# Performance work log

Measured on AMD Instinct MI355X. Metric: run time of the kernel, lower is better.

Reference implementation:

```python
import jax, jax.numpy as jnp
import numpy as np

B, N, M, C, T, HF, WF = 4, 512, 32, 512, 8, 14, 14
K = 80          # num_classes
P = 7           # ROI pool output size
HID = 1024
IMG = 224


def setup_inputs() -> dict:
    key = jax.random.key(0)
    k0, k1, k2, k3, k4, k5 = jax.random.split(key, 6)
    feature = jax.random.normal(k0, (B, C, T, HF, WF), dtype=jnp.float32)
    # GT boxes: realistic xyxy boxes inside a 224x224 image
    ka, kb = jax.random.split(k1)
    cxy = jax.random.uniform(ka, (B, M, 2), minval=40.0, maxval=180.0)
    wh = jax.random.uniform(kb, (B, M, 2), minval=40.0, maxval=100.0)
    gt_bboxes = jnp.concatenate([cxy - wh / 2, cxy + wh / 2], axis=-1).astype(jnp.float32)
    # Proposals: jittered copies of GT boxes so many pass the IoU>=0.85 fg test
    idx = jnp.arange(N) % M
    base = gt_bboxes[:, idx]                                   # [B,N,4]
    noise = jax.random.normal(k2, (B, N, 4), dtype=jnp.float32) * 1.5
    proposal_bboxes = jnp.clip(base + noise, 0.0, float(IMG))
    gt_classes = (jax.random.uniform(k3, (B, M, K)) < 0.1).astype(jnp.float32)
    W1 = jax.random.normal(k4, (C * P * P, HID), dtype=jnp.float32) * 0.01
    b1 = jnp.zeros((HID,), jnp.float32)
    W2 = jax.random.normal(k5, (HID, K), dtype=jnp.float32) * 0.01
    b2 = jnp.zeros((K,), jnp.float32)
    return {"feature": feature, "proposal_bboxes": proposal_bboxes,
            "gt_bboxes": gt_bboxes, "gt_classes": gt_classes,
            "W1": W1, "b1": b1, "W2": W2, "b2": b2,
            "image_h": IMG, "image_w": IMG}


def _iou(a, b):
    # a [B,N,4], b [B,M,4] xyxy -> [B,N,M]
    lt = jnp.maximum(a[:, :, None, :2], b[:, None, :, :2])
    rb = jnp.minimum(a[:, :, None, 2:], b[:, None, :, 2:])
    wh = jnp.clip(rb - lt, 0.0)
    inter = wh[..., 0] * wh[..., 1]
    area_a = (a[..., 2] - a[..., 0]) * (a[..., 3] - a[..., 1])
    area_b = (b[..., 2] - b[..., 0]) * (b[..., 3] - b[..., 1])
    return inter / (area_a[:, :, None] + area_b[:, None, :] - inter + 1e-8)


def _roi_pool(feat_bhwc, boxes, bidx, sy, sx):
    # feat_bhwc [B,H,W,C]; boxes [R,4] image coords; bilinear 7x7 ROI pooling
    H, W = feat_bhwc.shape[1], feat_bhwc.shape[2]
    x1, y1, x2, y2 = boxes[:, 0] * sx, boxes[:, 1] * sy, boxes[:, 2] * sx, boxes[:, 3] * sy
    g = (jnp.arange(P, dtype=jnp.float32) + 0.5) / P
    ys = y1[:, None] + g[None, :] * (y2 - y1)[:, None]        # [R,P]
    xs = x1[:, None] + g[None, :] * (x2 - x1)[:, None]        # [R,P]
    y = jnp.broadcast_to(ys[:, :, None], (boxes.shape[0], P, P)) - 0.5
    x = jnp.broadcast_to(xs[:, None, :], (boxes.shape[0], P, P)) - 0.5
    y0f = jnp.floor(y); x0f = jnp.floor(x)
    wy = jnp.clip(y - y0f, 0.0, 1.0)[..., None]
    wx = jnp.clip(x - x0f, 0.0, 1.0)[..., None]
    y0 = jnp.clip(y0f, 0, H - 1).astype(jnp.int32)
    y1i = jnp.clip(y0f + 1, 0, H - 1).astype(jnp.int32)
    x0 = jnp.clip(x0f, 0, W - 1).astype(jnp.int32)
    x1i = jnp.clip(x0f + 1, 0, W - 1).astype(jnp.int32)
    bi = bidx[:, None, None]
    gather = lambda yy, xx: feat_bhwc[bi, yy, xx]             # [R,P,P,C]
    out = (gather(y0, x0) * (1 - wy) * (1 - wx) + gather(y0, x1i) * (1 - wy) * wx +
           gather(y1i, x0) * wy * (1 - wx) + gather(y1i, x1i) * wy * wx)
    return out


def reference(feature, proposal_bboxes, gt_bboxes, gt_classes, W1, b1, W2, b2, image_h, image_w):
    # temporal average pool (AvgPool3d over T) -> [B,C,HF,WF]
    feat = feature.mean(axis=2)
    feat_bhwc = jnp.transpose(feat, (0, 2, 3, 1))             # [B,HF,WF,C]
    # IoU-based fg assignment
    ious = _iou(proposal_bboxes, gt_bboxes)                   # [B,N,M]
    max_iou = ious.max(axis=2)                                # [B,N]
    assign = ious.argmax(axis=2)                              # [B,N]
    any_fg = jnp.any(max_iou >= 0.85)
    thresh = jnp.where(any_fg, 0.85, 0.5)                     # fallback branch
    fg = (max_iou >= thresh).astype(feature.dtype)            # [B,N]
    # ROI pool all proposals (bg masked out in the loss)
    boxes = proposal_bboxes.reshape(B * N, 4)
    bidx = jnp.repeat(jnp.arange(B, dtype=jnp.int32), N)
    sy = feat.shape[2] / float(image_h)
    sx = feat.shape[3] / float(image_w)
    pool = _roi_pool(feat_bhwc, boxes, bidx, sy, sx)          # [R,P,P,C]
    pool = jnp.transpose(pool, (0, 3, 1, 2)).reshape(B * N, C * P * P)
    hidden = jax.nn.relu(pool @ W1 + b1)                      # [R,HID]
    logits = hidden @ W2 + b2                                 # [R,K]
    # multilabel soft-margin labels per proposal
    labels = gt_classes[jnp.repeat(jnp.arange(B), N), assign.reshape(-1)]  # [R,K]
    per = -(labels * jax.nn.log_sigmoid(logits) +
            (1.0 - labels) * jax.nn.log_sigmoid(-logits)).mean(axis=-1)    # [R]
    per = per.reshape(B, N)
    cnt = fg.sum(axis=1)
    losses = jnp.where(cnt > 0, (per * fg).sum(axis=1) / jnp.maximum(cnt, 1.0), 0.0)
    return losses
```

## Files before the change

### kernel.cpp

```cpp
#include <hip/hip_runtime.h>
#include <cstdint>
#include <cstddef>

#define KTOT 25088
#define NBOX 2048
#define HID  1024

typedef __bf16 bf16x8 __attribute__((ext_vector_type(8)));
typedef float  f32x4  __attribute__((ext_vector_type(4)));

__device__ __forceinline__ unsigned short f2bf(float f) {
  union { float f; unsigned u; } v; v.f = f;
  unsigned r = v.u + 0x7FFFu + ((v.u >> 16) & 1u);
  return (unsigned short)(r >> 16);
}

__device__ __forceinline__ float scalar_f(const void* p) {
  int iv = *(const int*)p;
  if (iv > 0 && iv < (1 << 20)) return (float)iv;
  return *(const float*)p;
}

__global__ __launch_bounds__(256) void k_meant(const float* __restrict__ feature,
                                               float* __restrict__ fbhwc) {
  int id = blockIdx.x * 256 + threadIdx.x;
  if (id >= 4 * 512 * 196) return;
  int pix = id % 196;
  int c   = (id / 196) & 511;
  int b   = id / (196 * 512);
  const float* p = feature + ((size_t)(b * 512 + c) * 8) * 196 + pix;
  float s = 0.f;
#pragma unroll
  for (int t = 0; t < 8; ++t) s += p[t * 196];
  fbhwc[((size_t)(b * 196 + pix)) * 512 + c] = s * 0.125f;
}

__global__ __launch_bounds__(256) void k_iou(const float* __restrict__ prop,
                                             const float* __restrict__ gtb,
                                             float* __restrict__ max_iou,
                                             int* __restrict__ assign,
                                             int* __restrict__ flag) {
  __shared__ float g[128];
  int gid = blockIdx.x * 256 + threadIdx.x;
  int b = gid >> 9;
  if (threadIdx.x < 128) g[threadIdx.x] = gtb[b * 128 + threadIdx.x];
  __syncthreads();
  float x1 = prop[gid * 4 + 0], y1 = prop[gid * 4 + 1];
  float x2 = prop[gid * 4 + 2], y2 = prop[gid * 4 + 3];
  float aa = (x2 - x1) * (y2 - y1);
  float best = -1e30f; int arg = 0;
  for (int m = 0; m < 32; ++m) {
    float gx1 = g[m*4], gy1 = g[m*4+1], gx2 = g[m*4+2], gy2 = g[m*4+3];
    float iw = fmaxf(fminf(x2, gx2) - fmaxf(x1, gx1), 0.f);
    float ih = fmaxf(fminf(y2, gy2) - fmaxf(y1, gy1), 0.f);
    float inter = iw * ih;
    float ab = (gx2 - gx1) * (gy2 - gy1);
    float iou = inter / (aa + ab - inter + 1e-8f);
    if (iou > best) { best = iou; arg = m; }
  }
  max_iou[gid] = best; assign[gid] = arg;
  if (best >= 0.85f) atomicOr(flag, 1);
}

__global__ __launch_bounds__(256) void k_w1t(const float* __restrict__ W1,
                                             unsigned short* __restrict__ W1T) {
  __shared__ unsigned short tile[64][68];
  int kp0 = blockIdx.x * 64;
  int h0  = blockIdx.y * 64;
  int t = threadIdx.x;
  int seg = t & 15, ro = t >> 4;
#pragma unroll
  for (int r = 0; r < 4; ++r) {
    int i = ro + r * 16;
    int kp = kp0 + i;
    int srow = (kp & 511) * 49 + (kp >> 9);
    float4 v = *(const float4*)(W1 + (size_t)srow * 1024 + h0 + seg * 4);
    tile[i][seg*4+0] = f2bf(v.x);
    tile[i][seg*4+1] = f2bf(v.y);
    tile[i][seg*4+2] = f2bf(v.z);
    tile[i][seg*4+3] = f2bf(v.w);
  }
  __syncthreads();
#pragma unroll
  for (int r = 0; r < 4; ++r) {
    int hi = ro + r * 16;
    unsigned a = tile[seg*4+0][hi];
    unsigned b = tile[seg*4+1][hi];
    unsigned c = tile[seg*4+2][hi];
    unsigned d = tile[seg*4+3][hi];
    *(uint2*)(W1T + (size_t)(h0+hi)*KTOT + kp0 + seg*4) =
        make_uint2(a | (b << 16), c | (d << 16));
  }
}

__global__ __launch_bounds__(256) void k_roipool(const float* __restrict__ fbhwc,
                                                 const float* __restrict__ prop,
                                                 const void* ihp, const void* iwp,
                                                 unsigned short* __restrict__ Apool) {
  int n = blockIdx.x;
  int tid = threadIdx.x;
  float sy = 14.f / scalar_f(ihp);
  float sx = 14.f / scalar_f(iwp);
  float bx1 = prop[n*4+0]*sx, by1 = prop[n*4+1]*sy;
  float bx2 = prop[n*4+2]*sx, by2 = prop[n*4+3]*sy;
  const float* fb = fbhwc + (size_t)(n >> 9) * 196 * 512;
  unsigned short* arow = Apool + (size_t)n * KTOT;
  int c4 = (tid & 127) << 2;
  int bh = tid >> 7;
  for (int b2i = 0; b2i < 49; b2i += 2) {
    int bin = b2i + bh;
    if (bin >= 49) continue;
    int py = bin / 7, px = bin - py * 7;
    float y = by1 + ((py + 0.5f) * (1.f/7.f)) * (by2 - by1) - 0.5f;
    float x = bx1 + ((px + 0.5f) * (1.f/7.f)) * (bx2 - bx1) - 0.5f;
    float y0f = floorf(y), x0f = floorf(x);
    float wy = y - y0f, wx = x - x0f;
    int y0  = min(max((int)y0f, 0), 13);
    int y1i = min(max((int)y0f + 1, 0), 13);
    int x0  = min(max((int)x0f, 0), 13);
    int x1i = min(max((int)x0f + 1, 0), 13);
    float w00 = (1.f - wy) * (1.f - wx), w01 = (1.f - wy) * wx;
    float w10 = wy * (1.f - wx),         w11 = wy * wx;
    const float4 f00 = *(const float4*)(fb + (y0 * 14 + x0 ) * 512 + c4);
    const float4 f01 = *(const float4*)(fb + (y0 * 14 + x1i) * 512 + c4);
    const float4 f10 = *(const float4*)(fb + (y1i * 14 + x0 ) * 512 + c4);
    const float4 f11 = *(const float4*)(fb + (y1i * 14 + x1i) * 512 + c4);
    float vx = f00.x*w00 + f01.x*w01 + f10.x*w10 + f11.x*w11;
    float vy = f00.y*w00 + f01.y*w01 + f10.y*w10 + f11.y*w11;
    float vz = f00.z*w00 + f01.z*w01 + f10.z*w10 + f11.z*w11;
    float vw = f00.w*w00 + f01.w*w01 + f10.w*w10 + f11.w*w11;
    unsigned lo = (unsigned)f2bf(vx) | ((unsigned)f2bf(vy) << 16);
    unsigned hi = (unsigned)f2bf(vz) | ((unsigned)f2bf(vw) << 16);
    *(uint2*)(arow + bin * 512 + c4) = make_uint2(lo, hi);
  }
}

__device__ __forceinline__ void gload16(const unsigned short* g, unsigned short* l) {
  __builtin_amdgcn_global_load_lds(
      (const __attribute__((address_space(1))) unsigned int*)g,
      (__attribute__((address_space(3))) unsigned int*)l, 16, 0, 0);
}

__global__ __launch_bounds__(512, 2) void k_gemm1(
    const unsigned short* __restrict__ A,
    const unsigned short* __restrict__ B,
    unsigned short* __restrict__ hp)
{
  extern __shared__ unsigned short lds[];
  const int tid  = threadIdx.x;
  const int w    = tid >> 6;
  const int lane = tid & 63;
  const int l15  = lane & 15;
  const int wr = w >> 2, wc = w & 3;
  const int bid = (int)blockIdx.x;
  const int wg  = (bid & 7) * 32 + (bid >> 3);
  const int kb  = wg >> 5;
  const int gy  = (wg >> 2) & 7;
  const int gx  = wg & 3;

  f32x4 acc[8][4];
  const f32x4 zero = {0.f, 0.f, 0.f, 0.f};
#pragma unroll
  for (int m = 0; m < 8; ++m)
#pragma unroll
    for (int n = 0; n < 4; ++n) acc[m][n] = zero;

  const int xsw  = (tid & 7) ^ ((tid >> 3) & 7);
  const int rloc = ((tid >> 3) << 1) + (xsw >> 2);
  const int qsrc = xsw & 3;
  const size_t kbase = (size_t)kb * 3136;
  const unsigned short* gAp = A + (size_t)(gy * 256 + rloc) * KTOT + kbase + qsrc * 8;
  const unsigned short* gBp = B + (size_t)(gx * 256 + rloc) * KTOT + kbase + qsrc * 8;
  const int dstc = tid * 8;

  const int pfr   = ((lane >> 4) | ((l15 & 1) << 2)) ^ (l15 >> 1);
  const int aoffc = wr * 4096 + (l15 >> 1) * 64 + pfr * 8;
  const int boffc = wc * 2048 + (l15 >> 1) * 64 + pfr * 8;

  bf16x8 af[8], b0[2], b1[2];

#define VMW2 asm volatile("s_waitcnt vmcnt(2)" ::: "memory");
#define VMW0 asm volatile("s_waitcnt vmcnt(0)" ::: "memory");
#define DSR_A(CB, UOFF) _Pragma("unroll") for (int m = 0; m < 8; ++m) \
    af[m] = *reinterpret_cast<const bf16x8*>(lds + (CB) + (UOFF) + aoffc + m * 512);
#define DSR_B(BV, CB, UOFF, NH) _Pragma("unroll") for (int nn = 0; nn < 2; ++nn) \
    BV[nn] = *reinterpret_cast<const bf16x8*>(lds + (CB) + (UOFF) + boffc + ((NH)*2+nn) * 512);
#define MM16(BV, NH) _Pragma("unroll") for (int m = 0; m < 8; ++m) \
    _Pragma("unroll") for (int nn = 0; nn < 2; ++nn) \
      acc[m][(NH)*2+nn] = __builtin_amdgcn_mfma_f32_16x16x32_bf16(af[m], BV[nn], acc[m][(NH)*2+nn], 0, 0, 0);
#define STG(OB, UOFF, GP, KOFF) { \
    gload16((GP) + (KOFF),                      lds + (OB) + (UOFF) + dstc); \
    gload16((GP) + (KOFF) + (size_t)128 * KTOT, lds + (OB) + (UOFF) + 4096 + dstc); }
#define PHTAIL \
    __builtin_amdgcn_sched_barrier(0); \
    __builtin_amdgcn_s_barrier(); \
    asm volatile("s_waitcnt lgkmcnt(0)" ::: "memory"); \
    __builtin_amdgcn_sched_barrier(0); \
    __builtin_amdgcn_s_setprio(1);
#define PHEND \
    __builtin_amdgcn_s_setprio(0); \
    __builtin_amdgcn_s_barrier();

#define KSTEP(CB, OB, KN, DOST, VM1C)                                          \
  {                                   \
    DSR_A(CB, 0)                                                               \
    DSR_B(b0, CB, 16384, 0)                                                    \
    if (DOST) STG(OB, 0, gAp, KN)                                              \
    PHTAIL  MM16(b0, 0)  PHEND                                                 \
                                          \
    VM1C                                                                       \
    DSR_B(b1, CB, 16384, 1)                                                    \
    if (DOST) STG(OB, 16384, gBp, KN)                                          \
    PHTAIL  MM16(b1, 1)  PHEND                                                 \
                                      \
    DSR_A(CB, 8192)                                                            \
    DSR_B(b0, CB, 24576, 0)                                                    \
    if (DOST) STG(OB, 8192, gAp, (KN) + 32)                                    \
    PHTAIL  MM16(b0, 0)  PHEND                                                 \
                                          \
    if (DOST) VMW2                                                             \
    DSR_B(b1, CB, 24576, 1)                                                    \
    if (DOST) STG(OB, 24576, gBp, (KN) + 32)                                   \
    PHTAIL  MM16(b1, 1)  PHEND                                                 \
  }

  STG(0, 0,     gAp, 0)
  STG(0, 16384, gBp, 0)
  STG(0, 8192,  gAp, 32)
  STG(0, 24576, gBp, 32)
  asm volatile("s_waitcnt vmcnt(4)" ::: "memory");
  __builtin_amdgcn_s_barrier();

#pragma unroll 1
  for (int s = 0; s < 48; s += 2) {
    const int kn1 = (s + 1) * 64;
    const int kn2 = (s + 2) * 64;
    KSTEP(0,     32768, kn1, true, VMW2)
    KSTEP(32768, 0,     kn2, true, VMW2)
  }
  KSTEP(0, 32768, 0, false, VMW0)

#undef KSTEP
#undef PHEND
#undef PHTAIL
#undef STG
#undef MM16
#undef DSR_B
#undef DSR_A
#undef VMW0
#undef VMW2

  unsigned short* o = hp + (size_t)kb * (2048u * 1024u);
  const int r0 = gy * 256 + wr * 128 + ((lane >> 4) << 2);
  const int c0 = gx * 256 + wc * 64 + l15;
#pragma unroll
  for (int m = 0; m < 8; ++m)
#pragma unroll
    for (int n = 0; n < 4; ++n)
#pragma unroll
      for (int j = 0; j < 4; ++j)
        o[(size_t)(r0 + m * 16 + j) * 1024 + c0 + n * 16] = f2bf(acc[m][n][j]);
}

template<int OUTBF>
__global__ __launch_bounds__(256, 4) void k_gemm(
    const unsigned short* __restrict__ A,
    const unsigned short* __restrict__ B,
    void* __restrict__ outp,
    int Kst, int kIters, int nTileBits, int mTileBits, int ldc)
{
  __shared__ unsigned short As[2][4096];
  __shared__ unsigned short Bs[2][4096];
  const int tid  = threadIdx.x;
  const int w    = tid >> 6;
  const int lane = tid & 63;
  const int nwg = (int)gridDim.x, cpx = nwg >> 3;
  const int bid = (int)blockIdx.x;
  const int wg  = (bid & 7) * cpx + (bid >> 3);
  const int kb  = wg >> (mTileBits + nTileBits);
  const int rem = wg & ((1 << (mTileBits + nTileBits)) - 1);
  const int gy  = rem >> nTileBits;
  const int gx  = rem & ((1 << nTileBits) - 1);
  const int wr = w >> 1, wc = w & 1;

  f32x4 acc[4][4];
  const f32x4 zero = {0.f, 0.f, 0.f, 0.f};
#pragma unroll
  for (int m = 0; m < 4; ++m)
#pragma unroll
    for (int n = 0; n < 4; ++n) acc[m][n] = zero;

  const int r0   = 32 * w + (lane >> 2);
  const int qsrc = (lane & 3) ^ ((lane >> 3) & 3);
  const size_t kbase = (size_t)kb * kIters * 32;
  const unsigned short* gA = A + (size_t)(gy * 128 + r0) * Kst + kbase + qsrc * 8;
  const unsigned short* gB = B + (size_t)(gx * 128 + r0) * Kst + kbase + qsrc * 8;
  const int ldst = r0 * 32 + (lane & 3) * 8;

  const int swq = ((lane >> 4) ^ ((lane >> 1) & 3)) * 8;
  const int ar = (wr * 64 + (lane & 15)) * 32 + swq;
  const int br = (wc * 64 + (lane & 15)) * 32 + swq;

#define STAGE(bufi, it) do {                                         \
    const unsigned short* pa = gA + (size_t)(it) * 32;               \
    const unsigned short* pb = gB + (size_t)(it) * 32;               \
    gload16(pa,                      &As[bufi][ldst]);               \
    gload16(pa + (size_t)16 * Kst,   &As[bufi][ldst + 512]);         \
    gload16(pb,                      &Bs[bufi][ldst]);               \
    gload16(pb + (size_t)16 * Kst,   &Bs[bufi][ldst + 512]);         \
  } while (0)

  STAGE(0, 0);
  int cur = 0;
  for (int kk = 0; kk < kIters; ++kk) {
    __syncthreads();
    if (kk + 1 < kIters) STAGE(cur ^ 1, kk + 1);
    bf16x8 af[4], bfr[4];
#pragma unroll
    for (int m = 0; m < 4; ++m)
      af[m] = *reinterpret_cast<const bf16x8*>(&As[cur][ar + m * 512]);
#pragma unroll
    for (int n = 0; n < 4; ++n)
      bfr[n] = *reinterpret_cast<const bf16x8*>(&Bs[cur][br + n * 512]);
#pragma unroll
    for (int m = 0; m < 4; ++m)
#pragma unroll
      for (int n = 0; n < 4; ++n)
        acc[m][n] = __builtin_amdgcn_mfma_f32_16x16x32_bf16(af[m], bfr[n], acc[m][n], 0, 0, 0);
    cur ^= 1;
  }
#undef STAGE

  const size_t M = (size_t)(1 << mTileBits) * 128;
  const size_t splitStride = M * (size_t)ldc;
  const int r0o = gy * 128 + wr * 64 + ((lane >> 4) << 2);
  const int c0o = gx * 128 + wc * 64 + (lane & 15);
  if (OUTBF) {
    unsigned short* o = (unsigned short*)outp + (size_t)kb * splitStride;
#pragma unroll
    for (int m = 0; m < 4; ++m)
#pragma unroll
      for (int n = 0; n < 4; ++n)
#pragma unroll
        for (int j = 0; j < 4; ++j)
          o[(size_t)(r0o + m * 16 + j) * ldc + c0o + n * 16] = f2bf(acc[m][n][j]);
  } else {
    float* o = (float*)outp + (size_t)kb * splitStride;
#pragma unroll
    for (int m = 0; m < 4; ++m)
#pragma unroll
      for (int n = 0; n < 4; ++n)
#pragma unroll
        for (int j = 0; j < 4; ++j)
          o[(size_t)(r0o + m * 16 + j) * ldc + c0o + n * 16] = acc[m][n][j];
  }
}

__global__ __launch_bounds__(256) void k_combine(const unsigned short* __restrict__ hp,
                                                 const float* __restrict__ b1,
                                                 unsigned short* __restrict__ hidden) {
  int gid = blockIdx.x * 256 + threadIdx.x;
  int id8 = gid * 8;
  int h = id8 & 1023;
  float a[8];
#pragma unroll
  for (int j = 0; j < 8; ++j) a[j] = b1[h + j];
#pragma unroll
  for (int s = 0; s < 8; ++s) {
    uint4 u = *(const uint4*)(hp + (size_t)s * 2097152 + id8);
    unsigned uu[4] = {u.x, u.y, u.z, u.w};
#pragma unroll
    for (int q = 0; q < 4; ++q) {
      union { unsigned u; float f; } lo, hi;
      lo.u = uu[q] << 16; hi.u = uu[q] & 0xFFFF0000u;
      a[2*q]   += lo.f;
      a[2*q+1] += hi.f;
    }
  }
  unsigned out[4];
#pragma unroll
  for (int q = 0; q < 4; ++q) {
    unsigned l  = f2bf(fmaxf(a[2*q],   0.f));
    unsigned hh = f2bf(fmaxf(a[2*q+1], 0.f));
    out[q] = l | (hh << 16);
  }
  *(uint4*)(hidden + id8) = make_uint4(out[0], out[1], out[2], out[3]);
}

__global__ __launch_bounds__(256) void k_w2t(const float* __restrict__ W2,
                                             unsigned short* __restrict__ W2T) {
  int id = blockIdx.x * 256 + threadIdx.x;
  int cls = id >> 10, k = id & 1023;
  float v = (cls < 80) ? W2[(size_t)k * 80 + cls] : 0.f;
  W2T[id] = f2bf(v);
}

__global__ __launch_bounds__(256) void k_bce(const float* __restrict__ hp2,
                                             const float* __restrict__ b2,
                                             const float* __restrict__ gtc,
                                             const int* __restrict__ assign,
                                             float* __restrict__ per) {
  __shared__ float red[256];
  int t = threadIdx.x;
  int box = t >> 4, li = t & 15;
  int n = blockIdx.x * 16 + box;
  int lab = ((n >> 9) * 32 + assign[n]) * 80;
  float s = 0.f;
#pragma unroll
  for (int j = 0; j < 5; ++j) {
    int c = li + 16 * j;
    size_t o = (size_t)n * 128 + c;
    float x = hp2[o] + hp2[o + 262144] + hp2[o + 524288] + hp2[o + 786432] + b2[c];
    float y = gtc[lab + c];
    float ce = log1pf(expf(-fabsf(x)));
    s += y * (fmaxf(-x, 0.f) + ce) + (1.f - y) * (fmaxf(x, 0.f) + ce);
  }
  red[t] = s;
  __syncthreads();
  if (li == 0) {
    float tot = 0.f;
#pragma unroll
    for (int i = 0; i < 16; ++i) tot += red[box * 16 + i];
    per[n] = tot * (1.f / 80.f);
  }
}

__global__ __launch_bounds__(512) void k_reduce(const float* __restrict__ per,
                                                const float* __restrict__ max_iou,
                                                const int* __restrict__ flag,
                                                float* __restrict__ out) {
  __shared__ float sv[8], sf[8];
  int b = blockIdx.x, tid = threadIdx.x;
  float thr = (*flag) ? 0.85f : 0.5f;
  int n = b * 512 + tid;
  float f = (max_iou[n] >= thr) ? 1.f : 0.f;
  float v = per[n] * f;
#pragma unroll
  for (int o = 32; o > 0; o >>= 1) {
    v += __shfl_down(v, o);
    f += __shfl_down(f, o);
  }
  int wv = tid >> 6;
  if ((tid & 63) == 0) { sv[wv] = v; sf[wv] = f; }
  __syncthreads();
  if (tid == 0) {
    float S = 0.f, F = 0.f;
#pragma unroll
    for (int i = 0; i < 8; ++i) { S += sv[i]; F += sf[i]; }
    out[b] = (F > 0.f) ? S / fmaxf(F, 1.f) : 0.f;
  }
}

extern "C" void kernel_launch(void* const* d_in, const int* in_sizes, int n_in,
                              void* d_out, int out_size, void* d_ws, size_t ws_size,
                              hipStream_t stream) {
  const float* feature = (const float*)d_in[0];
  const float* prop    = (const float*)d_in[1];
  const float* gtb     = (const float*)d_in[2];
  const float* gtc     = (const float*)d_in[3];
  const float* W1      = (const float*)d_in[4];
  const float* b1      = (const float*)d_in[5];
  const float* W2      = (const float*)d_in[6];
  const float* b2      = (const float*)d_in[7];
  const void*  ihp     = d_in[8];
  const void*  iwp     = d_in[9];

  char* ws = (char*)d_ws;
  float*          fbhwc  = (float*)(ws);
  unsigned short* W1T    = (unsigned short*)(ws + 1605632);
  unsigned short* Apool  = (unsigned short*)(ws + 52985856);
  unsigned short* hp     = (unsigned short*)(ws + 155746304);
  float*          max_iou= (float*)(ws + 189300736);
  int*            assign = (int*)(ws + 189308928);
  float*          per    = (float*)(ws + 189317120);
  int*            flag   = (int*)(ws + 189325312);
  unsigned short* hidden = W1T;
  unsigned short* W2T    = Apool;
  float*          hp2    = (float*)((char*)Apool + 262144);

  hipFuncSetAttribute((const void*)k_gemm1,
                      hipFuncAttributeMaxDynamicSharedMemorySize, 131072);

  hipMemsetAsync(flag, 0, sizeof(int), stream);
  k_meant  <<<1568, 256, 0, stream>>>(feature, fbhwc);
  k_iou    <<<8, 256, 0, stream>>>(prop, gtb, max_iou, assign, flag);
  k_w1t    <<<dim3(392, 16), 256, 0, stream>>>(W1, W1T);
  k_roipool<<<2048, 256, 0, stream>>>(fbhwc, prop, ihp, iwp, Apool);
  k_gemm1  <<<256, 512, 131072, stream>>>(Apool, W1T, hp);
  k_combine<<<1024, 256, 0, stream>>>(hp, b1, hidden);
  k_w2t    <<<512, 256, 0, stream>>>(W2, W2T);
  k_gemm<0><<<64, 256, 0, stream>>>(hidden, W2T, hp2, 1024, 8, 0, 4, 128);
  k_bce    <<<128, 256, 0, stream>>>(hp2, b2, gtc, assign, per);
  k_reduce <<<4, 512, 0, stream>>>(per, max_iou, flag, (float*)d_out);
}
```

Before: 196.9 us.

## Restructure split-K GEMM mainloop into four-stage LDS ring with half-tile phases

```diff
diff --git a/kernel.cpp b/kernel.cpp
--- a/kernel.cpp
+++ b/kernel.cpp
@@ -177,78 +177,76 @@
   const int aoffc = wr * 4096 + (l15 >> 1) * 64 + pfr * 8;
   const int boffc = wc * 2048 + (l15 >> 1) * 64 + pfr * 8;
 
-  bf16x8 af[8], b0[2], b1[2];
-
-#define VMW2 asm volatile("s_waitcnt vmcnt(2)" ::: "memory");
-#define VMW0 asm volatile("s_waitcnt vmcnt(0)" ::: "memory");
-#define DSR_A(CB, UOFF) _Pragma("unroll") for (int m = 0; m < 8; ++m) \
-    af[m] = *reinterpret_cast<const bf16x8*>(lds + (CB) + (UOFF) + aoffc + m * 512);
-#define DSR_B(BV, CB, UOFF, NH) _Pragma("unroll") for (int nn = 0; nn < 2; ++nn) \
-    BV[nn] = *reinterpret_cast<const bf16x8*>(lds + (CB) + (UOFF) + boffc + ((NH)*2+nn) * 512);
-#define MM16(BV, NH) _Pragma("unroll") for (int m = 0; m < 8; ++m) \
-    _Pragma("unroll") for (int nn = 0; nn < 2; ++nn) \
-      acc[m][(NH)*2+nn] = __builtin_amdgcn_mfma_f32_16x16x32_bf16(af[m], BV[nn], acc[m][(NH)*2+nn], 0, 0, 0);
-#define STG(OB, UOFF, GP, KOFF) { \
-    gload16((GP) + (KOFF),                      lds + (OB) + (UOFF) + dstc); \
-    gload16((GP) + (KOFF) + (size_t)128 * KTOT, lds + (OB) + (UOFF) + 4096 + dstc); }
-#define PHTAIL \
+  bf16x8 af[4], bfr[4];
+
+#define STGA(OB, KN) { \
+    gload16(gAp + (KN),                      lds + (OB) + dstc); \
+    gload16(gAp + (KN) + (size_t)128 * KTOT, lds + (OB) + 4096 + dstc); }
+#define STGB(OB, KN) { \
+    gload16(gBp + (KN),                      lds + (OB) + 8192 + dstc); \
+    gload16(gBp + (KN) + (size_t)128 * KTOT, lds + (OB) + 12288 + dstc); }
+#define DSRA(CB, MB) _Pragma("unroll") for (int i = 0; i < 4; ++i) \
+    af[i] = *reinterpret_cast<const bf16x8*>(lds + (CB) + aoffc + ((MB) + i) * 512);
+#define DSRB(CB) _Pragma("unroll") for (int n = 0; n < 4; ++n) \
+    bfr[n] = *reinterpret_cast<const bf16x8*>(lds + (CB) + 8192 + boffc + n * 512);
+#define MMQ(MH) _Pragma("unroll") for (int i = 0; i < 4; ++i) \
+    _Pragma("unroll") for (int n = 0; n < 4; ++n) \
+      acc[(MH)*4 + i][n] = __builtin_amdgcn_mfma_f32_16x16x32_bf16( \
+          af[i], bfr[n], acc[(MH)*4 + i][n], 0, 0, 0);
+#define PHX \
     __builtin_amdgcn_sched_barrier(0); \
     __builtin_amdgcn_s_barrier(); \
     asm volatile("s_waitcnt lgkmcnt(0)" ::: "memory"); \
     __builtin_amdgcn_sched_barrier(0); \
     __builtin_amdgcn_s_setprio(1);
-#define PHEND \
-    __builtin_amdgcn_s_setprio(0); \
-    __builtin_amdgcn_s_barrier();
-
-#define KSTEP(CB, OB, KN, DOST, VM1C)                                          \
-  {                                   \
-    DSR_A(CB, 0)                                                               \
-    DSR_B(b0, CB, 16384, 0)                                                    \
-    if (DOST) STG(OB, 0, gAp, KN)                                              \
-    PHTAIL  MM16(b0, 0)  PHEND                                                 \
-                                          \
-    VM1C                                                                       \
-    DSR_B(b1, CB, 16384, 1)                                                    \
-    if (DOST) STG(OB, 16384, gBp, KN)                                          \
-    PHTAIL  MM16(b1, 1)  PHEND                                                 \
-                                      \
-    DSR_A(CB, 8192)                                                            \
-    DSR_B(b0, CB, 24576, 0)                                                    \
-    if (DOST) STG(OB, 8192, gAp, (KN) + 32)                                    \
-    PHTAIL  MM16(b0, 0)  PHEND                                                 \
-                                          \
-    if (DOST) VMW2                                                             \
-    DSR_B(b1, CB, 24576, 1)                                                    \
-    if (DOST) STG(OB, 24576, gBp, (KN) + 32)                                   \
-    PHTAIL  MM16(b1, 1)  PHEND                                                 \
-  }
-
-  STG(0, 0,     gAp, 0)
-  STG(0, 16384, gBp, 0)
-  STG(0, 8192,  gAp, 32)
-  STG(0, 24576, gBp, 32)
-  asm volatile("s_waitcnt vmcnt(4)" ::: "memory");
+#define VM4 asm volatile("s_waitcnt vmcnt(4)" ::: "memory");
+#define VM0 asm volatile("s_waitcnt vmcnt(0)" ::: "memory");
+#define VMN
+
+#define KSTEP(CB, OB, KN, DOST, VME)                                          \
+  {                                                   \
+    DSRA(CB, 0)                                                               \
+    DSRB(CB)                                                                  \
+    if (DOST) STGA(OB, KN)                                                    \
+    PHX  MMQ(0)                                                               \
+    __builtin_amdgcn_s_setprio(0);                                            \
+    __builtin_amdgcn_s_barrier();                                             \
+                        \
+    DSRA(CB, 4)                                                               \
+    DSRB(CB)                                                                  \
+    if (DOST) STGB(OB, KN)                                                    \
+    PHX  MMQ(1)                                                               \
+    __builtin_amdgcn_s_setprio(0);                                            \
+    VME                                                                       \
+    __builtin_amdgcn_s_barrier();                                             \
+  }
+
+  STGA(0, 0)      STGB(0, 0)
+  STGA(16384, 32) STGB(16384, 32)
+  VM4
   __builtin_amdgcn_s_barrier();
 
 #pragma unroll 1
-  for (int s = 0; s < 48; s += 2) {
-    const int kn1 = (s + 1) * 64;
-    const int kn2 = (s + 2) * 64;
-    KSTEP(0,     32768, kn1, true, VMW2)
-    KSTEP(32768, 0,     kn2, true, VMW2)
-  }
-  KSTEP(0, 32768, 0, false, VMW0)
+  for (int sq = 0; sq < 96; sq += 4) {
+    const int kn = (sq + 2) * 32;
+    KSTEP(0,     32768, kn,      true, VM4)
+    KSTEP(16384, 49152, kn + 32, true, VM4)
+    KSTEP(32768, 0,     kn + 64, true, VM4)
+    KSTEP(49152, 16384, kn + 96, true, VM4)
+  }
+  KSTEP(0,     0, 0, false, VM0)
+  KSTEP(16384, 0, 0, false, VMN)
 
 #undef KSTEP
-#undef PHEND
-#undef PHTAIL
-#undef STG
-#undef MM16
-#undef DSR_B
-#undef DSR_A
-#undef VMW0
-#undef VMW2
+#undef VMN
+#undef VM0
+#undef VM4
+#undef PHX
+#undef MMQ
+#undef DSRB
+#undef DSRA
+#undef STGB
+#undef STGA
 
   unsigned short* o = hp + (size_t)kb * (2048u * 1024u);
   const int r0 = gy * 256 + wr * 128 + ((lane >> 4) << 2);
```

Measured after the change: 203.0 us. +3.1%, slower.
